# Kernel optimization log

Hardware: AMD Instinct MI355X
Metric: run time of the kernel (lower is better)

The kernel has to match this reference:

```python
import jax, jax.numpy as jnp
import numpy as np

D_MODEL = 3072
N_HEADS = 24
HEAD_DIM = D_MODEL // N_HEADS          # 128
Q_PROJ = D_MODEL // 2                  # 1536
KV_PROJ = 2 * D_MODEL // 3             # 2048
ROPE_DIM = HEAD_DIM // 2               # 64 (qk_rope_dim == qk_no_rope_dim)
MAX_LEN = 2048
ROPE_THETA = 10000.0
EPS = 1e-6
B, S = 2, 2048


def setup_inputs() -> dict:
    key = jax.random.key(0)
    ks = jax.random.split(key, 7)
    return {
        "x": jax.random.normal(ks[0], (B, S, D_MODEL), dtype=jnp.float32),
        "scale": jnp.ones((D_MODEL,), dtype=jnp.float32),
        "w_dq": 0.01 * jax.random.normal(ks[1], (D_MODEL, Q_PROJ), dtype=jnp.float32),
        "w_uq": 0.01 * jax.random.normal(ks[2], (Q_PROJ, D_MODEL), dtype=jnp.float32),
        "w_dkv": 0.01 * jax.random.normal(ks[3], (D_MODEL, KV_PROJ + ROPE_DIM), dtype=jnp.float32),
        "w_ukv": 0.01 * jax.random.normal(ks[4], (KV_PROJ, D_MODEL + N_HEADS * ROPE_DIM), dtype=jnp.float32),
        "w_o": 0.01 * jax.random.normal(ks[5], (D_MODEL, D_MODEL), dtype=jnp.float32),
    }


def _rope_cos_sin(seq_len):
    # freqs over full head_dim, sliced to rope_dim//2 then tiled x2 (as in torch repeat)
    freqs = 1.0 / (ROPE_THETA ** (jnp.arange(0, HEAD_DIM, 2, dtype=jnp.float32) / HEAD_DIM))
    angles = jnp.arange(seq_len, dtype=jnp.float32)[:, None] * freqs[None, :]  # [S, 64]
    ang = angles[:, : ROPE_DIM // 2]                                            # [S, 32]
    cos = jnp.tile(jnp.cos(ang), (1, 2))                                        # [S, 64]
    sin = jnp.tile(jnp.sin(ang), (1, 2))
    return cos[None, None], sin[None, None]  # [1,1,S,64]


def _rotate_half(t):
    a, b = jnp.split(t, 2, axis=-1)
    return jnp.concatenate([-b, a], axis=-1)


def reference(x, scale, w_dq, w_uq, w_dkv, w_ukv, w_o):
    b, s, _ = x.shape
    # RMSNorm pre-normalization
    xn = scale * (x * jax.lax.rsqrt(jnp.mean(x * x, axis=-1, keepdims=True) + EPS))
    # two-stage query projection
    q = (xn @ w_dq) @ w_uq                                   # [B,S,D]
    q = q.reshape(b, s, N_HEADS, HEAD_DIM).transpose(0, 2, 1, 3)  # [B,H,S,hd]
    q_no_rope, q_rope = jnp.split(q, [ROPE_DIM], axis=-1)
    cos, sin = _rope_cos_sin(s)
    q_rope = q_rope * cos + _rotate_half(q_rope) * sin
    # KV down projection (this is the kv cache)
    kv_down = xn @ w_dkv                                     # [B,S,KV_PROJ+rope]
    kv_no_rope, k_rope = jnp.split(kv_down, [KV_PROJ], axis=-1)
    # KV up projection
    kv_up = kv_no_rope @ w_ukv                               # [B,S,H*(hd+rope)]
    kv_up = kv_up.reshape(b, s, N_HEADS, HEAD_DIM + ROPE_DIM).transpose(0, 2, 1, 3)
    key, value = jnp.split(kv_up, [ROPE_DIM], axis=-1)       # key [B,H,S,64], value [B,H,S,128]
    # shared rope key (one head, broadcast to all heads)
    k_rope = k_rope[:, None, :, :]                           # [B,1,S,64]
    k_rope = k_rope * cos + _rotate_half(k_rope) * sin
    k_rope = jnp.broadcast_to(k_rope, (b, N_HEADS, s, ROPE_DIM))
    final_q = jnp.concatenate([q_no_rope, q_rope], axis=-1)  # [B,H,S,128]
    final_k = jnp.concatenate([key, k_rope], axis=-1)        # [B,H,S,128]
    # masked SDPA (causal, past_length=0)
    inv_scale = 1.0 / jnp.sqrt(jnp.asarray(HEAD_DIM, dtype=x.dtype))
    scores = jnp.einsum("bhsd,bhtd->bhst", final_q, final_k) * inv_scale
    causal = jnp.tril(jnp.ones((s, s), dtype=bool))
    scores = jnp.where(causal[None, None], scores, jnp.asarray(-1e30, dtype=scores.dtype))
    attn = jax.nn.softmax(scores, axis=-1)
    attn_out = jnp.einsum("bhst,bhtd->bhsd", attn, value)    # [B,H,S,128]
    attn_out = attn_out.transpose(0, 2, 1, 3).reshape(b, s, D_MODEL)
    output = attn_out @ w_o.T
    return output, kv_down
```

## Files before the change

kernel.cpp:

```cpp
#include <hip/hip_runtime.h>
#include <hip/hip_bf16.h>
#include <stdint.h>

using bf16_t = __bf16;
using bf16x8 = __attribute__((ext_vector_type(8))) __bf16;
using bf16x4 = __attribute__((ext_vector_type(4))) __bf16;
using f32x4  = __attribute__((ext_vector_type(4))) float;

#define D_MODEL 3072
#define N_HEADS 24
#define HEAD_DIM 128
#define Q_PROJ 1536
#define KV_PROJ 2048
#define ROPE_DIM 64
#define S_LEN 2048
#define NTOK 4096
#define KVDN 2112
#define KVUN 4608

__device__ __forceinline__ void async_ld16(const void* g, void* l) {
    __builtin_amdgcn_global_load_lds(
        (__attribute__((address_space(1))) uint32_t*)(uintptr_t)g,
        (__attribute__((address_space(3))) uint32_t*)(uint32_t)(uintptr_t)l,
        16, 0, 0);
}

#define BARRIER() __builtin_amdgcn_s_barrier()
#define WAITV4() asm volatile("s_waitcnt vmcnt(4)" ::: "memory")
#define WAITV0() asm volatile("s_waitcnt vmcnt(0)" ::: "memory")

__global__ __launch_bounds__(256) void rmsnorm_kernel(
    const float* __restrict__ x, const float* __restrict__ sc, bf16_t* __restrict__ xn)
{
    const int tok = blockIdx.x;
    const int t = threadIdx.x;
    const float4* xr = (const float4*)(x + (size_t)tok * D_MODEL);
    float4 a = xr[t], b = xr[t + 256], c = xr[t + 512];
    float ss = a.x*a.x + a.y*a.y + a.z*a.z + a.w*a.w
             + b.x*b.x + b.y*b.y + b.z*b.z + b.w*b.w
             + c.x*c.x + c.y*c.y + c.z*c.z + c.w*c.w;
    #pragma unroll
    for (int off = 32; off >= 1; off >>= 1) ss += __shfl_xor(ss, off);
    __shared__ float red[4];
    if ((t & 63) == 0) red[t >> 6] = ss;
    __syncthreads();
    const float inv = rsqrtf((red[0] + red[1] + red[2] + red[3]) * (1.0f / D_MODEL) + 1e-6f);
    const float4* sr = (const float4*)sc;
    float4 s0 = sr[t], s1 = sr[t + 256], s2 = sr[t + 512];
    bf16x4* xo = (bf16x4*)(xn + (size_t)tok * D_MODEL);
    bf16x4 o;
    o[0]=(bf16_t)(a.x*s0.x*inv); o[1]=(bf16_t)(a.y*s0.y*inv); o[2]=(bf16_t)(a.z*s0.z*inv); o[3]=(bf16_t)(a.w*s0.w*inv);
    xo[t] = o;
    o[0]=(bf16_t)(b.x*s1.x*inv); o[1]=(bf16_t)(b.y*s1.y*inv); o[2]=(bf16_t)(b.z*s1.z*inv); o[3]=(bf16_t)(b.w*s1.w*inv);
    xo[t + 256] = o;
    o[0]=(bf16_t)(c.x*s2.x*inv); o[1]=(bf16_t)(c.y*s2.y*inv); o[2]=(bf16_t)(c.z*s2.z*inv); o[3]=(bf16_t)(c.w*s2.w*inv);
    xo[t + 512] = o;
}

__global__ void transpose_conv(const float* __restrict__ in, bf16_t* __restrict__ out, int K, int N)
{
    __shared__ float tile[32][33];
    const int n0 = blockIdx.x * 32, k0 = blockIdx.y * 32;
    const int tx = threadIdx.x, ty = threadIdx.y;
    #pragma unroll
    for (int i = 0; i < 32; i += 8)
        tile[ty + i][tx] = in[(size_t)(k0 + ty + i) * N + n0 + tx];
    __syncthreads();
    #pragma unroll
    for (int i = 0; i < 32; i += 8)
        out[(size_t)(n0 + ty + i) * K + k0 + tx] = (bf16_t)tile[tx][ty + i];
}

__global__ void conv_bf16(const float* __restrict__ in, bf16_t* __restrict__ out, int n4)
{
    const int stride = gridDim.x * 256;
    for (int i = blockIdx.x * 256 + threadIdx.x; i < n4; i += stride) {
        float4 v = ((const float4*)in)[i];
        bf16x4 o;
        o[0] = (bf16_t)v.x; o[1] = (bf16_t)v.y; o[2] = (bf16_t)v.z; o[3] = (bf16_t)v.w;
        ((bf16x4*)out)[i] = o;
    }
}

template<int CFP>
__device__ __forceinline__ void mfma16(f32x4 (&acc)[8][4], const bf16x8 (&af)[8],
                                       const bf16x8 (&bfv)[2]) {
    __builtin_amdgcn_s_setprio(1);
    #pragma unroll
    for (int rf = 0; rf < 8; ++rf) {
        acc[rf][2*CFP]   = __builtin_amdgcn_mfma_f32_16x16x32_bf16(af[rf], bfv[0], acc[rf][2*CFP],   0, 0, 0);
        acc[rf][2*CFP+1] = __builtin_amdgcn_mfma_f32_16x16x32_bf16(af[rf], bfv[1], acc[rf][2*CFP+1], 0, 0, 0);
    }
    __builtin_amdgcn_s_setprio(0);
}

__global__ __launch_bounds__(512, 2) void gemm256(
    const bf16_t* __restrict__ A, const bf16_t* __restrict__ B, int N, int K,
    float* __restrict__ Cf, int ldf, int flo, int fhi,
    bf16_t* __restrict__ Cb1, int ldb1, int b1lo, int b1hi,
    bf16_t* __restrict__ Cb2, int ldb2, int b2lo, int b2hi)
{
    __shared__ char LDS[131072];
    char* Lc = LDS;
    const int tid = threadIdx.x;
    const int wv = tid >> 6, lane = tid & 63;
    const int fr = lane & 15, fg = lane >> 4;
    const int wr = wv >> 2, wc = wv & 3;
    const int m0 = blockIdx.y << 8, n0 = blockIdx.x << 8;
    const uint32_t slot4 = (uint32_t)((fg ^ ((fr >> 1) & 3)) << 4);

    int grow[2], gcol[2];
    const bf16_t* agp[2]; const bf16_t* bgp[2];
    uint32_t aoff[2], boff[2];
    #pragma unroll
    for (int j = 0; j < 2; ++j) {
        const int c = j * 512 + tid;
        const int g = c ^ ((c >> 3) & 3);
        grow[j] = g >> 2; gcol[j] = g & 3;
        agp[j] = A + (size_t)(m0 + grow[j]) * K + gcol[j] * 8;
        int br = n0 + grow[j]; if (br > N - 1) br = N - 1;
        bgp[j] = B + (size_t)br * K + gcol[j] * 8;
        aoff[j] = (uint32_t)((j * 8 + wv) * 1024);
        boff[j] = (uint32_t)(65536 + (j * 8 + wv) * 1024);
    }

    f32x4 acc[8][4];
    f32x4 zero = {0.f, 0.f, 0.f, 0.f};
    #pragma unroll
    for (int i = 0; i < 8; ++i)
        #pragma unroll
        for (int j = 0; j < 4; ++j) acc[i][j] = zero;

    bf16x8 af[8], bfv[2];
    const int rowA = (wr << 7) + fr;
    const int rowB = (wc << 6) + fr;

    auto stA = [&](int t, int kh) {
        const uint32_t sb = (uint32_t)(((2*t + kh) & 3) << 14);
        #pragma unroll
        for (int j = 0; j < 2; ++j)
            async_ld16(agp[j] + t * 64 + kh * 32, Lc + sb + aoff[j]);
    };
    auto stB = [&](int t, int kh) {
        const uint32_t sb = (uint32_t)(((2*t + kh) & 3) << 14);
        #pragma unroll
        for (int j = 0; j < 2; ++j)
            async_ld16(bgp[j] + t * 64 + kh * 32, Lc + sb + boff[j]);
    };
    auto ldA8 = [&](int t, int kh) {
        const uint32_t base = (uint32_t)(((2*t + kh) & 3) << 14);
        #pragma unroll
        for (int rf = 0; rf < 8; ++rf)
            af[rf] = *(const bf16x8*)(Lc + base + (rowA + rf * 16) * 64 + slot4);
    };
    auto ldB2 = [&](int t, int kh, int cfp) {
        const uint32_t base = (uint32_t)(65536 + (((2*t + kh) & 3) << 14));
        #pragma unroll
        for (int c = 0; c < 2; ++c)
            bfv[c] = *(const bf16x8*)(Lc + base + (rowB + (cfp * 2 + c) * 16) * 64 + slot4);
    };

    const int NT = K >> 6, nIter = NT >> 1;
    stA(0, 0); stB(0, 0); stA(0, 1); stB(0, 1); stA(1, 0); stB(1, 0);
    WAITV4(); BARRIER();

    for (int i = 0; i < nIter; ++i) {
        const int t0 = 2 * i, t1 = t0 + 1, t2 = t0 + 2, t3 = t0 + 3;
        const bool pref = (i < nIter - 1);
        ldA8(t0, 0); ldB2(t0, 0, 0); stA(t1, 1);
        BARRIER(); mfma16<0>(acc, af, bfv); BARRIER();
        ldB2(t0, 0, 1); stB(t1, 1);
        BARRIER(); mfma16<1>(acc, af, bfv); BARRIER();
        ldA8(t0, 1); ldB2(t0, 1, 0); if (pref) stA(t2, 0);
        BARRIER(); mfma16<0>(acc, af, bfv); BARRIER();
        ldB2(t0, 1, 1); if (pref) stB(t2, 0);
        if (pref) { WAITV4(); } else { WAITV0(); }
        BARRIER(); mfma16<1>(acc, af, bfv); BARRIER();
        ldA8(t1, 0); ldB2(t1, 0, 0); if (pref) stA(t2, 1);
        BARRIER(); mfma16<0>(acc, af, bfv); BARRIER();
        ldB2(t1, 0, 1); if (pref) stB(t2, 1);
        BARRIER(); mfma16<1>(acc, af, bfv); BARRIER();
        ldA8(t1, 1); ldB2(t1, 1, 0); if (pref) stA(t3, 0);
        BARRIER(); mfma16<0>(acc, af, bfv); BARRIER();
        ldB2(t1, 1, 1); if (pref) stB(t3, 0);
        WAITV4();
        BARRIER(); mfma16<1>(acc, af, bfv); BARRIER();
    }

    const int colb = n0 + (wc << 6) + fr;
    const int rowb = m0 + (wr << 7) + fg * 4;
    #pragma unroll
    for (int rf = 0; rf < 8; ++rf)
        #pragma unroll
        for (int cf = 0; cf < 4; ++cf) {
            const int col = colb + cf * 16;
            #pragma unroll
            for (int r = 0; r < 4; ++r) {
                const int row = rowb + rf * 16 + r;
                const float v = acc[rf][cf][r];
                if (Cf  && col >= flo  && col < fhi)  Cf [(size_t)row * ldf  + col - flo]  = v;
                if (Cb1 && col >= b1lo && col < b1hi) Cb1[(size_t)row * ldb1 + col - b1lo] = (bf16_t)v;
                if (Cb2 && col >= b2lo && col < b2hi) Cb2[(size_t)row * ldb2 + col - b2lo] = (bf16_t)v;
            }
        }
}

__global__ void rope_tab(float* __restrict__ ctab, float* __restrict__ stab)
{
    const int idx = blockIdx.x * 256 + threadIdx.x;
    if (idx >= S_LEN * 32) return;
    const int s = idx >> 5, i = idx & 31;
    const float freq = powf(10000.0f, -(float)(2 * i) * (1.0f / 128.0f));
    const float ang = (float)s * freq;
    ctab[idx] = cosf(ang);
    stab[idx] = sinf(ang);
}

__global__ void rope_q_kernel(bf16_t* __restrict__ q, const float* __restrict__ ctab,
                              const float* __restrict__ stab)
{
    const int idx = blockIdx.x * 256 + threadIdx.x;
    if (idx >= NTOK * N_HEADS * 32) return;
    const int i = idx & 31;
    const int rest = idx >> 5;
    const int h = rest % N_HEADS;
    const int tok = rest / N_HEADS;
    const int s = tok & (S_LEN - 1);
    bf16_t* p = q + (size_t)tok * D_MODEL + h * HEAD_DIM + 64;
    const float a = (float)p[i], b = (float)p[i + 32];
    const float c = ctab[s * 32 + i], sn = stab[s * 32 + i];
    p[i]      = (bf16_t)(a * c - b * sn);
    p[i + 32] = (bf16_t)(b * c + a * sn);
}

__global__ void rope_k_kernel(const float* __restrict__ kvd, bf16_t* __restrict__ kr,
                              const float* __restrict__ ctab, const float* __restrict__ stab)
{
    const int idx = blockIdx.x * 256 + threadIdx.x;
    if (idx >= NTOK * 32) return;
    const int i = idx & 31;
    const int tok = idx >> 5;
    const int s = tok & (S_LEN - 1);
    const float* p = kvd + (size_t)tok * KVDN + KV_PROJ;
    const float a = p[i], b = p[i + 32];
    const float c = ctab[s * 32 + i], sn = stab[s * 32 + i];
    kr[(size_t)tok * 64 + i]      = (bf16_t)(a * c - b * sn);
    kr[(size_t)tok * 64 + i + 32] = (bf16_t)(b * c + a * sn);
}

__global__ void vt_asm(const bf16_t* __restrict__ kvup, bf16_t* __restrict__ vt)
{
    __shared__ bf16_t tile[32][33];
    const int s0 = blockIdx.x * 32, d0 = blockIdx.y * 32, bh = blockIdx.z;
    const int b = bh / N_HEADS, h = bh % N_HEADS;
    const int tx = threadIdx.x, ty = threadIdx.y;
    #pragma unroll
    for (int i = 0; i < 32; i += 8)
        tile[ty + i][tx] = kvup[(size_t)(b * S_LEN + s0 + ty + i) * KVUN + h * 192 + 64 + d0 + tx];
    __syncthreads();
    #pragma unroll
    for (int i = 0; i < 32; i += 8)
        vt[((size_t)bh * HEAD_DIM + d0 + ty + i) * S_LEN + s0 + tx] = tile[tx][ty + i];
}

__global__ __launch_bounds__(256, 2) void attn_fwd(
    const bf16_t* __restrict__ Q, const bf16_t* __restrict__ KVUP,
    const bf16_t* __restrict__ KR, const bf16_t* __restrict__ VT,
    bf16_t* __restrict__ AO)
{
    __shared__ bf16_t Knr[64 * 64];
    __shared__ bf16_t Krp[64 * 64];
    __shared__ bf16_t Vls[128 * 64];
    __shared__ bf16_t Pls[4 * 32 * 72];

    const int bh = blockIdx.y;
    const int b = bh / N_HEADS, h = bh % N_HEADS;
    const int wave = threadIdx.x >> 6, lane = threadIdx.x & 63;
    const int fr = lane & 15, fg = lane >> 4;
    const int rx = fr & 7;

    const bf16_t* Kb  = KVUP + (size_t)b * S_LEN * KVUN + (size_t)h * 192;
    const bf16_t* KRb = KR + (size_t)b * S_LEN * 64;
    const bf16_t* Vb  = VT + (size_t)bh * HEAD_DIM * S_LEN;
    bf16_t* P = Pls + wave * (32 * 72);

    const int srow   = lane >> 3;
    const int schunk = (lane & 7) ^ srow;
    const float l2e_isc = 0.127500625f;

    f32x4 zero = {0.f, 0.f, 0.f, 0.f};

    #pragma unroll 1
    for (int tp = 0; tp < 2; ++tp) {
        const int qt = (tp == 0) ? blockIdx.x : (15 - blockIdx.x);
        const int qb = qt * 128;
        const int wrow0 = qb + wave * 32;

        bf16x8 qf[2][4];
        #pragma unroll
        for (int rf = 0; rf < 2; ++rf)
            #pragma unroll
            for (int kc = 0; kc < 4; ++kc)
                qf[rf][kc] = *(const bf16x8*)(Q + (size_t)(b * S_LEN + wrow0 + rf * 16 + fr) * D_MODEL
                                              + h * HEAD_DIM + kc * 32 + fg * 8);
        f32x4 oacc[2][8];
        float m_i[2][4], l_i[2][4];
        #pragma unroll
        for (int rf = 0; rf < 2; ++rf) {
            #pragma unroll
            for (int nf = 0; nf < 8; ++nf) oacc[rf][nf] = zero;
            #pragma unroll
            for (int r = 0; r < 4; ++r) { m_i[rf][r] = -1e30f; l_i[rf][r] = 0.f; }
        }

        const int kvend = qb + 128;
        #pragma unroll 1
        for (int kvb = 0; kvb < kvend; kvb += 64) {
            __syncthreads();
            #pragma unroll
            for (int c = 0; c < 2; ++c) {
                const int r0 = wave * 16 + c * 8;
                async_ld16(Kb  + (size_t)(kvb + r0 + srow) * KVUN + schunk * 8, Knr + r0 * 64);
                async_ld16(KRb + (size_t)(kvb + r0 + srow) * 64   + schunk * 8, Krp + r0 * 64);
            }
            #pragma unroll
            for (int c = 0; c < 4; ++c) {
                const int r0 = wave * 32 + c * 8;
                async_ld16(Vb + (size_t)(r0 + srow) * S_LEN + kvb + schunk * 8, Vls + r0 * 64);
            }
            __syncthreads();

            if (kvb > wrow0 + 31) continue;

            f32x4 sacc[2][4];
            #pragma unroll
            for (int rf = 0; rf < 2; ++rf)
                #pragma unroll
                for (int jn = 0; jn < 4; ++jn) sacc[rf][jn] = zero;
            #pragma unroll
            for (int jn = 0; jn < 4; ++jn) {
                const int krow = jn * 16 + fr;
                bf16x8 kA = *(const bf16x8*)(Knr + krow * 64 + (((0 + fg) ^ rx) << 3));
                bf16x8 kB = *(const bf16x8*)(Knr + krow * 64 + (((4 + fg) ^ rx) << 3));
                bf16x8 kC = *(const bf16x8*)(Krp + krow * 64 + (((0 + fg) ^ rx) << 3));
                bf16x8 kD = *(const bf16x8*)(Krp + krow * 64 + (((4 + fg) ^ rx) << 3));
                #pragma unroll
                for (int rf = 0; rf < 2; ++rf) {
                    sacc[rf][jn] = __builtin_amdgcn_mfma_f32_16x16x32_bf16(qf[rf][0], kA, sacc[rf][jn], 0, 0, 0);
                    sacc[rf][jn] = __builtin_amdgcn_mfma_f32_16x16x32_bf16(qf[rf][1], kB, sacc[rf][jn], 0, 0, 0);
                    sacc[rf][jn] = __builtin_amdgcn_mfma_f32_16x16x32_bf16(qf[rf][2], kC, sacc[rf][jn], 0, 0, 0);
                    sacc[rf][jn] = __builtin_amdgcn_mfma_f32_16x16x32_bf16(qf[rf][3], kD, sacc[rf][jn], 0, 0, 0);
                }
            }

            const bool needMask = (kvb + 63 > wrow0);
            float mrow[2][4];
            #pragma unroll
            for (int rf = 0; rf < 2; ++rf)
                #pragma unroll
                for (int r = 0; r < 4; ++r) {
                    const int row = wrow0 + rf * 16 + fg * 4 + r;
                    float mx = -1e30f;
                    #pragma unroll
                    for (int jn = 0; jn < 4; ++jn) {
                        float v = sacc[rf][jn][r] * l2e_isc;
                        if (needMask && (kvb + jn * 16 + fr > row)) v = -1e30f;
                        sacc[rf][jn][r] = v;
                        mx = fmaxf(mx, v);
                    }
                    mrow[rf][r] = mx;
                }
            #pragma unroll
            for (int off = 1; off < 16; off <<= 1)
                #pragma unroll
                for (int rf = 0; rf < 2; ++rf)
                    #pragma unroll
                    for (int r = 0; r < 4; ++r)
                        mrow[rf][r] = fmaxf(mrow[rf][r], __shfl_xor(mrow[rf][r], off));
            float scf[2][4], lsum[2][4];
            #pragma unroll
            for (int rf = 0; rf < 2; ++rf)
                #pragma unroll
                for (int r = 0; r < 4; ++r) {
                    const float mn = fmaxf(m_i[rf][r], mrow[rf][r]);
                    scf[rf][r] = __builtin_amdgcn_exp2f(m_i[rf][r] - mn);
                    m_i[rf][r] = mn;
                    float s = 0.f;
                    #pragma unroll
                    for (int jn = 0; jn < 4; ++jn) {
                        const float p = __builtin_amdgcn_exp2f(sacc[rf][jn][r] - mn);
                        sacc[rf][jn][r] = p;
                        s += p;
                    }
                    lsum[rf][r] = s;
                }
            #pragma unroll
            for (int off = 1; off < 16; off <<= 1)
                #pragma unroll
                for (int rf = 0; rf < 2; ++rf)
                    #pragma unroll
                    for (int r = 0; r < 4; ++r)
                        lsum[rf][r] += __shfl_xor(lsum[rf][r], off);
            #pragma unroll
            for (int rf = 0; rf < 2; ++rf)
                #pragma unroll
                for (int r = 0; r < 4; ++r) {
                    l_i[rf][r] = l_i[rf][r] * scf[rf][r] + lsum[rf][r];
                    #pragma unroll
                    for (int nf = 0; nf < 8; ++nf) oacc[rf][nf][r] *= scf[rf][r];
                }

            #pragma unroll
            for (int rf = 0; rf < 2; ++rf)
                #pragma unroll
                for (int jn = 0; jn < 4; ++jn)
                    #pragma unroll
                    for (int r = 0; r < 4; ++r)
                        P[(rf * 16 + fg * 4 + r) * 72 + jn * 16 + fr] = (bf16_t)sacc[rf][jn][r];
            bf16x8 pf[2][2];
            #pragma unroll
            for (int rf = 0; rf < 2; ++rf)
                #pragma unroll
                for (int c = 0; c < 2; ++c)
                    pf[rf][c] = *(const bf16x8*)(P + (rf * 16 + fr) * 72 + c * 32 + fg * 8);

            #pragma unroll
            for (int nf = 0; nf < 8; ++nf) {
                const int vrow = nf * 16 + fr;
                bf16x8 v0 = *(const bf16x8*)(Vls + vrow * 64 + (((0 + fg) ^ rx) << 3));
                bf16x8 v1 = *(const bf16x8*)(Vls + vrow * 64 + (((4 + fg) ^ rx) << 3));
                #pragma unroll
                for (int rf = 0; rf < 2; ++rf) {
                    oacc[rf][nf] = __builtin_amdgcn_mfma_f32_16x16x32_bf16(pf[rf][0], v0, oacc[rf][nf], 0, 0, 0);
                    oacc[rf][nf] = __builtin_amdgcn_mfma_f32_16x16x32_bf16(pf[rf][1], v1, oacc[rf][nf], 0, 0, 0);
                }
            }
        }

        #pragma unroll
        for (int rf = 0; rf < 2; ++rf) {
            float rl[4];
            #pragma unroll
            for (int r = 0; r < 4; ++r) rl[r] = __builtin_amdgcn_rcpf(l_i[rf][r]);
            #pragma unroll
            for (int nf = 0; nf < 8; ++nf)
                #pragma unroll
                for (int r = 0; r < 4; ++r) {
                    const int row = wrow0 + rf * 16 + fg * 4 + r;
                    AO[(size_t)(b * S_LEN + row) * D_MODEL + h * HEAD_DIM + nf * 16 + fr] =
                        (bf16_t)(oacc[rf][nf][r] * rl[r]);
                }
        }
    }
}

extern "C" void kernel_launch(void* const* d_in, const int* in_sizes, int n_in,
                              void* d_out, int out_size, void* d_ws, size_t ws_size,
                              hipStream_t stream)
{
    const float* x     = (const float*)d_in[0];
    const float* scale = (const float*)d_in[1];
    const float* w_dq  = (const float*)d_in[2];
    const float* w_uq  = (const float*)d_in[3];
    const float* w_dkv = (const float*)d_in[4];
    const float* w_ukv = (const float*)d_in[5];
    const float* w_o   = (const float*)d_in[6];
    float* out0 = (float*)d_out;
    float* out1 = out0 + (size_t)NTOK * D_MODEL;

    if (ws_size < 187039744ull) return;
    char* ws = (char*)d_ws;
    bf16_t* XN    = (bf16_t*)(ws + 0);
    bf16_t* WCAT  = (bf16_t*)(ws + 25165824ull);
    bf16_t* WUQT  = (bf16_t*)(ws + 47579136ull);
    bf16_t* WUKVT = (bf16_t*)(ws + 57016320ull);
    bf16_t* WOB   = (bf16_t*)(ws + 75890688ull);
    bf16_t* QD    = (bf16_t*)(ws + 94765056ull);
    bf16_t* Qb    = (bf16_t*)(ws + 107347968ull);
    bf16_t* KVNR  = (bf16_t*)(ws + 132513792ull);
    bf16_t* KVUP  = (bf16_t*)(ws + 149291008ull);
    bf16_t* KRB   = (bf16_t*)(ws + 94765056ull);
    float*  CTAB  = (float*) (ws + 95289344ull);
    float*  STAB  = (float*) (ws + 95551488ull);
    bf16_t* VTb   = WCAT;
    bf16_t* AO    = XN;

    rmsnorm_kernel<<<NTOK, 256, 0, stream>>>(x, scale, XN);
    transpose_conv<<<dim3(1536/32, 3072/32), dim3(32,8), 0, stream>>>(w_dq,  WCAT, 3072, 1536);
    transpose_conv<<<dim3(2112/32, 3072/32), dim3(32,8), 0, stream>>>(w_dkv, WCAT + (size_t)1536*3072, 3072, 2112);
    transpose_conv<<<dim3(3072/32, 1536/32), dim3(32,8), 0, stream>>>(w_uq,  WUQT, 1536, 3072);
    transpose_conv<<<dim3(4608/32, 2048/32), dim3(32,8), 0, stream>>>(w_ukv, WUKVT, 2048, 4608);
    conv_bf16<<<2048, 256, 0, stream>>>(w_o, WOB, (D_MODEL * D_MODEL) / 4);

    gemm256<<<dim3(15, 16), 512, 0, stream>>>(XN, WCAT, 3648, 3072,
        out1, KVDN, 1536, 3648,
        QD,   Q_PROJ, 0, 1536,
        KVNR, KV_PROJ, 1536, 3584);
    gemm256<<<dim3(12, 16), 512, 0, stream>>>(QD, WUQT, 3072, 1536,
        nullptr, 0, 0, 0, Qb, D_MODEL, 0, 3072, nullptr, 0, 0, 0);
    rope_tab<<<(S_LEN * 32 + 255) / 256, 256, 0, stream>>>(CTAB, STAB);
    rope_q_kernel<<<(NTOK * N_HEADS * 32 + 255) / 256, 256, 0, stream>>>(Qb, CTAB, STAB);
    rope_k_kernel<<<(NTOK * 32 + 255) / 256, 256, 0, stream>>>(out1, KRB, CTAB, STAB);
    gemm256<<<dim3(18, 16), 512, 0, stream>>>(KVNR, WUKVT, 4608, 2048,
        nullptr, 0, 0, 0, KVUP, KVUN, 0, 4608, nullptr, 0, 0, 0);
    vt_asm<<<dim3(S_LEN/32, HEAD_DIM/32, 48), dim3(32,8), 0, stream>>>(KVUP, VTb);
    attn_fwd<<<dim3(8, 48), 256, 0, stream>>>(Qb, KVUP, KRB, VTb, AO);
    gemm256<<<dim3(12, 16), 512, 0, stream>>>(AO, WOB, 3072, 3072,
        out0, D_MODEL, 0, 3072, nullptr, 0, 0, 0, nullptr, 0, 0, 0);
}
```

Before: 590.8 us.

## Double-buffer KV tiles and transpose MFMA to keep P in registers

Makes the attention kernel double-buffer its K, rope-K and V LDS tiles, so the async load of the next block overlaps compute on the current one and one barrier per iteration is removed. It swaps the MFMA operand order so scores come out transposed: each lane then owns one query row, the row max and sum need only two cross-lane shuffles, and P is passed to the PV MFMA through register shuffles instead of an LDS round trip. Output stores become 4-wide vectors. The cost is double the K/V LDS footprint and extra register pressure and shuffle work, which may reduce occupancy.

```diff
diff --git a/kernel.cpp b/kernel.cpp
--- a/kernel.cpp
+++ b/kernel.cpp
@@ -268,21 +268,22 @@
     const bf16_t* __restrict__ KR, const bf16_t* __restrict__ VT,
     bf16_t* __restrict__ AO)
 {
-    __shared__ bf16_t Knr[64 * 64];
-    __shared__ bf16_t Krp[64 * 64];
-    __shared__ bf16_t Vls[128 * 64];
-    __shared__ bf16_t Pls[4 * 32 * 72];
+    __shared__ bf16_t Knr[2][64 * 64];
+    __shared__ bf16_t Krp[2][64 * 64];
+    __shared__ bf16_t Vls[2][128 * 64];
 
     const int bh = blockIdx.y;
     const int b = bh / N_HEADS, h = bh % N_HEADS;
     const int wave = threadIdx.x >> 6, lane = threadIdx.x & 63;
     const int fr = lane & 15, fg = lane >> 4;
     const int rx = fr & 7;
+    const int hi = fg >> 1;
+    const int s0l = fr + 32 * (fg & 1);
+    const int s1l = s0l + 16;
 
     const bf16_t* Kb  = KVUP + (size_t)b * S_LEN * KVUN + (size_t)h * 192;
     const bf16_t* KRb = KR + (size_t)b * S_LEN * 64;
     const bf16_t* Vb  = VT + (size_t)bh * HEAD_DIM * S_LEN;
-    bf16_t* P = Pls + wave * (32 * 72);
 
     const int srow   = lane >> 3;
     const int schunk = (lane & 7) ^ srow;
@@ -304,152 +305,157 @@
                 qf[rf][kc] = *(const bf16x8*)(Q + (size_t)(b * S_LEN + wrow0 + rf * 16 + fr) * D_MODEL
                                               + h * HEAD_DIM + kc * 32 + fg * 8);
         f32x4 oacc[2][8];
-        float m_i[2][4], l_i[2][4];
+        float m_i[2], l_i[2];
         #pragma unroll
         for (int rf = 0; rf < 2; ++rf) {
             #pragma unroll
             for (int nf = 0; nf < 8; ++nf) oacc[rf][nf] = zero;
-            #pragma unroll
-            for (int r = 0; r < 4; ++r) { m_i[rf][r] = -1e30f; l_i[rf][r] = 0.f; }
+            m_i[rf] = -1e30f; l_i[rf] = 0.f;
         }
 
-        const int kvend = qb + 128;
-        #pragma unroll 1
-        for (int kvb = 0; kvb < kvend; kvb += 64) {
-            __syncthreads();
+        auto stage = [&](int kvb, int bf) {
             #pragma unroll
             for (int c = 0; c < 2; ++c) {
                 const int r0 = wave * 16 + c * 8;
-                async_ld16(Kb  + (size_t)(kvb + r0 + srow) * KVUN + schunk * 8, Knr + r0 * 64);
-                async_ld16(KRb + (size_t)(kvb + r0 + srow) * 64   + schunk * 8, Krp + r0 * 64);
+                async_ld16(Kb  + (size_t)(kvb + r0 + srow) * KVUN + schunk * 8, &Knr[bf][r0 * 64]);
+                async_ld16(KRb + (size_t)(kvb + r0 + srow) * 64   + schunk * 8, &Krp[bf][r0 * 64]);
             }
             #pragma unroll
             for (int c = 0; c < 4; ++c) {
                 const int r0 = wave * 32 + c * 8;
-                async_ld16(Vb + (size_t)(r0 + srow) * S_LEN + kvb + schunk * 8, Vls + r0 * 64);
+                async_ld16(Vb + (size_t)(r0 + srow) * S_LEN + kvb + schunk * 8, &Vls[bf][r0 * 64]);
+            }
+        };
+
+        const int kvend = qb + 128;
+        int cur = 0;
+        stage(0, 0);
+        __syncthreads();
+
+        #pragma unroll 1
+        for (int kvb = 0; kvb < kvend; kvb += 64) {
+            if (kvb + 64 < kvend) stage(kvb + 64, cur ^ 1);
+
+            if (kvb <= wrow0 + 31) {
+                const bf16_t* Kc = Knr[cur];
+                const bf16_t* Rc = Krp[cur];
+                const bf16_t* Vc = Vls[cur];
+
+                f32x4 sacc[2][4];
+                #pragma unroll
+                for (int rf = 0; rf < 2; ++rf)
+                    #pragma unroll
+                    for (int jn = 0; jn < 4; ++jn) sacc[rf][jn] = zero;
+                #pragma unroll
+                for (int jn = 0; jn < 4; ++jn) {
+                    const int krow = jn * 16 + fr;
+                    bf16x8 kA = *(const bf16x8*)(Kc + krow * 64 + (((0 + fg) ^ rx) << 3));
+                    bf16x8 kB = *(const bf16x8*)(Kc + krow * 64 + (((4 + fg) ^ rx) << 3));
+                    bf16x8 kC = *(const bf16x8*)(Rc + krow * 64 + (((0 + fg) ^ rx) << 3));
+                    bf16x8 kD = *(const bf16x8*)(Rc + krow * 64 + (((4 + fg) ^ rx) << 3));
+                    #pragma unroll
+                    for (int rf = 0; rf < 2; ++rf) {
+                        sacc[rf][jn] = __builtin_amdgcn_mfma_f32_16x16x32_bf16(kA, qf[rf][0], sacc[rf][jn], 0, 0, 0);
+                        sacc[rf][jn] = __builtin_amdgcn_mfma_f32_16x16x32_bf16(kB, qf[rf][1], sacc[rf][jn], 0, 0, 0);
+                        sacc[rf][jn] = __builtin_amdgcn_mfma_f32_16x16x32_bf16(kC, qf[rf][2], sacc[rf][jn], 0, 0, 0);
+                        sacc[rf][jn] = __builtin_amdgcn_mfma_f32_16x16x32_bf16(kD, qf[rf][3], sacc[rf][jn], 0, 0, 0);
+                    }
+                }
+
+                const bool needMask = (kvb + 63 > wrow0);
+                uint32_t pk[2][4][2];
+                float scf[2];
+                #pragma unroll
+                for (int rf = 0; rf < 2; ++rf) {
+                    const int qrow = wrow0 + rf * 16 + fr;
+                    float mx = -1e30f;
+                    #pragma unroll
+                    for (int jn = 0; jn < 4; ++jn)
+                        #pragma unroll
+                        for (int r = 0; r < 4; ++r) {
+                            float v = sacc[rf][jn][r] * l2e_isc;
+                            if (needMask && (kvb + jn * 16 + fg * 4 + r > qrow)) v = -1e30f;
+                            sacc[rf][jn][r] = v;
+                            mx = fmaxf(mx, v);
+                        }
+                    mx = fmaxf(mx, __shfl_xor(mx, 16));
+                    mx = fmaxf(mx, __shfl_xor(mx, 32));
+                    const float mn = fmaxf(m_i[rf], mx);
+                    scf[rf] = __builtin_amdgcn_exp2f(m_i[rf] - mn);
+                    m_i[rf] = mn;
+                    float ls = 0.f;
+                    #pragma unroll
+                    for (int jn = 0; jn < 4; ++jn) {
+                        float p0 = __builtin_amdgcn_exp2f(sacc[rf][jn][0] - mn);
+                        float p1 = __builtin_amdgcn_exp2f(sacc[rf][jn][1] - mn);
+                        float p2 = __builtin_amdgcn_exp2f(sacc[rf][jn][2] - mn);
+                        float p3 = __builtin_amdgcn_exp2f(sacc[rf][jn][3] - mn);
+                        ls += (p0 + p1) + (p2 + p3);
+                        union { bf16x4 h; uint32_t w[2]; } cv;
+                        cv.h[0] = (bf16_t)p0; cv.h[1] = (bf16_t)p1;
+                        cv.h[2] = (bf16_t)p2; cv.h[3] = (bf16_t)p3;
+                        pk[rf][jn][0] = cv.w[0]; pk[rf][jn][1] = cv.w[1];
+                    }
+                    ls += __shfl_xor(ls, 16);
+                    ls += __shfl_xor(ls, 32);
+                    l_i[rf] = l_i[rf] * scf[rf] + ls;
+                    #pragma unroll
+                    for (int nf = 0; nf < 8; ++nf)
+                        #pragma unroll
+                        for (int r = 0; r < 4; ++r) oacc[rf][nf][r] *= scf[rf];
+                }
+
+                bf16x8 bfr[2][2];
+                #pragma unroll
+                for (int rf = 0; rf < 2; ++rf)
+                    #pragma unroll
+                    for (int ks = 0; ks < 2; ++ks) {
+                        const uint32_t t00 = __shfl(pk[rf][2*ks][0],   s0l);
+                        const uint32_t t01 = __shfl(pk[rf][2*ks][1],   s0l);
+                        const uint32_t t10 = __shfl(pk[rf][2*ks+1][0], s0l);
+                        const uint32_t t11 = __shfl(pk[rf][2*ks+1][1], s0l);
+                        const uint32_t u00 = __shfl(pk[rf][2*ks][0],   s1l);
+                        const uint32_t u01 = __shfl(pk[rf][2*ks][1],   s1l);
+                        const uint32_t u10 = __shfl(pk[rf][2*ks+1][0], s1l);
+                        const uint32_t u11 = __shfl(pk[rf][2*ks+1][1], s1l);
+                        union { bf16x8 h; uint32_t w[4]; } bb;
+                        bb.w[0] = hi ? t10 : t00;
+                        bb.w[1] = hi ? t11 : t01;
+                        bb.w[2] = hi ? u10 : u00;
+                        bb.w[3] = hi ? u11 : u01;
+                        bfr[rf][ks] = bb.h;
+                    }
+
+                #pragma unroll
+                for (int nf = 0; nf < 8; ++nf) {
+                    const int vrow = nf * 16 + fr;
+                    bf16x8 v0 = *(const bf16x8*)(Vc + vrow * 64 + (((0 + fg) ^ rx) << 3));
+                    bf16x8 v1 = *(const bf16x8*)(Vc + vrow * 64 + (((4 + fg) ^ rx) << 3));
+                    #pragma unroll
+                    for (int rf = 0; rf < 2; ++rf) {
+                        oacc[rf][nf] = __builtin_amdgcn_mfma_f32_16x16x32_bf16(v0, bfr[rf][0], oacc[rf][nf], 0, 0, 0);
+                        oacc[rf][nf] = __builtin_amdgcn_mfma_f32_16x16x32_bf16(v1, bfr[rf][1], oacc[rf][nf], 0, 0, 0);
+                    }
+                }
             }
             __syncthreads();
-
-            if (kvb > wrow0 + 31) continue;
-
-            f32x4 sacc[2][4];
-            #pragma unroll
-            for (int rf = 0; rf < 2; ++rf)
-                #pragma unroll
-                for (int jn = 0; jn < 4; ++jn) sacc[rf][jn] = zero;
-            #pragma unroll
-            for (int jn = 0; jn < 4; ++jn) {
-                const int krow = jn * 16 + fr;
-                bf16x8 kA = *(const bf16x8*)(Knr + krow * 64 + (((0 + fg) ^ rx) << 3));
-                bf16x8 kB = *(const bf16x8*)(Knr + krow * 64 + (((4 + fg) ^ rx) << 3));
-                bf16x8 kC = *(const bf16x8*)(Krp + krow * 64 + (((0 + fg) ^ rx) << 3));
-                bf16x8 kD = *(const bf16x8*)(Krp + krow * 64 + (((4 + fg) ^ rx) << 3));
-                #pragma unroll
-                for (int rf = 0; rf < 2; ++rf) {
-                    sacc[rf][jn] = __builtin_amdgcn_mfma_f32_16x16x32_bf16(qf[rf][0], kA, sacc[rf][jn], 0, 0, 0);
-                    sacc[rf][jn] = __builtin_amdgcn_mfma_f32_16x16x32_bf16(qf[rf][1], kB, sacc[rf][jn], 0, 0, 0);
-                    sacc[rf][jn] = __builtin_amdgcn_mfma_f32_16x16x32_bf16(qf[rf][2], kC, sacc[rf][jn], 0, 0, 0);
-                    sacc[rf][jn] = __builtin_amdgcn_mfma_f32_16x16x32_bf16(qf[rf][3], kD, sacc[rf][jn], 0, 0, 0);
-                }
-            }
-
-            const bool needMask = (kvb + 63 > wrow0);
-            float mrow[2][4];
-            #pragma unroll
-            for (int rf = 0; rf < 2; ++rf)
-                #pragma unroll
-                for (int r = 0; r < 4; ++r) {
-                    const int row = wrow0 + rf * 16 + fg * 4 + r;
-                    float mx = -1e30f;
-                    #pragma unroll
-                    for (int jn = 0; jn < 4; ++jn) {
-                        float v = sacc[rf][jn][r] * l2e_isc;
-                        if (needMask && (kvb + jn * 16 + fr > row)) v = -1e30f;
-                        sacc[rf][jn][r] = v;
-                        mx = fmaxf(mx, v);
-                    }
-                    mrow[rf][r] = mx;
-                }
-            #pragma unroll
-            for (int off = 1; off < 16; off <<= 1)
-                #pragma unroll
-                for (int rf = 0; rf < 2; ++rf)
-                    #pragma unroll
-                    for (int r = 0; r < 4; ++r)
-                        mrow[rf][r] = fmaxf(mrow[rf][r], __shfl_xor(mrow[rf][r], off));
-            float scf[2][4], lsum[2][4];
-            #pragma unroll
-            for (int rf = 0; rf < 2; ++rf)
-                #pragma unroll
-                for (int r = 0; r < 4; ++r) {
-                    const float mn = fmaxf(m_i[rf][r], mrow[rf][r]);
-                    scf[rf][r] = __builtin_amdgcn_exp2f(m_i[rf][r] - mn);
-                    m_i[rf][r] = mn;
-                    float s = 0.f;
-                    #pragma unroll
-                    for (int jn = 0; jn < 4; ++jn) {
-                        const float p = __builtin_amdgcn_exp2f(sacc[rf][jn][r] - mn);
-                        sacc[rf][jn][r] = p;
-                        s += p;
-                    }
-                    lsum[rf][r] = s;
-                }
-            #pragma unroll
-            for (int off = 1; off < 16; off <<= 1)
-                #pragma unroll
-                for (int rf = 0; rf < 2; ++rf)
-                    #pragma unroll
-                    for (int r = 0; r < 4; ++r)
-                        lsum[rf][r] += __shfl_xor(lsum[rf][r], off);
-            #pragma unroll
-            for (int rf = 0; rf < 2; ++rf)
-                #pragma unroll
-                for (int r = 0; r < 4; ++r) {
-                    l_i[rf][r] = l_i[rf][r] * scf[rf][r] + lsum[rf][r];
-                    #pragma unroll
-                    for (int nf = 0; nf < 8; ++nf) oacc[rf][nf][r] *= scf[rf][r];
-                }
-
-            #pragma unroll
-            for (int rf = 0; rf < 2; ++rf)
-                #pragma unroll
-                for (int jn = 0; jn < 4; ++jn)
-                    #pragma unroll
-                    for (int r = 0; r < 4; ++r)
-                        P[(rf * 16 + fg * 4 + r) * 72 + jn * 16 + fr] = (bf16_t)sacc[rf][jn][r];
-            bf16x8 pf[2][2];
-            #pragma unroll
-            for (int rf = 0; rf < 2; ++rf)
-                #pragma unroll
-                for (int c = 0; c < 2; ++c)
-                    pf[rf][c] = *(const bf16x8*)(P + (rf * 16 + fr) * 72 + c * 32 + fg * 8);
-
+            cur ^= 1;
+        }
+
+        #pragma unroll
+        for (int rf = 0; rf < 2; ++rf) {
+            const float rl = __builtin_amdgcn_rcpf(l_i[rf]);
+            const int qrow = wrow0 + rf * 16 + fr;
+            bf16_t* aob = AO + (size_t)(b * S_LEN + qrow) * D_MODEL + h * HEAD_DIM + fg * 4;
             #pragma unroll
             for (int nf = 0; nf < 8; ++nf) {
-                const int vrow = nf * 16 + fr;
-                bf16x8 v0 = *(const bf16x8*)(Vls + vrow * 64 + (((0 + fg) ^ rx) << 3));
-                bf16x8 v1 = *(const bf16x8*)(Vls + vrow * 64 + (((4 + fg) ^ rx) << 3));
-                #pragma unroll
-                for (int rf = 0; rf < 2; ++rf) {
-                    oacc[rf][nf] = __builtin_amdgcn_mfma_f32_16x16x32_bf16(pf[rf][0], v0, oacc[rf][nf], 0, 0, 0);
-                    oacc[rf][nf] = __builtin_amdgcn_mfma_f32_16x16x32_bf16(pf[rf][1], v1, oacc[rf][nf], 0, 0, 0);
-                }
+                bf16x4 o;
+                o[0] = (bf16_t)(oacc[rf][nf][0] * rl);
+                o[1] = (bf16_t)(oacc[rf][nf][1] * rl);
+                o[2] = (bf16_t)(oacc[rf][nf][2] * rl);
+                o[3] = (bf16_t)(oacc[rf][nf][3] * rl);
+                *(bf16x4*)(aob + nf * 16) = o;
             }
-        }
-
-        #pragma unroll
-        for (int rf = 0; rf < 2; ++rf) {
-            float rl[4];
-            #pragma unroll
-            for (int r = 0; r < 4; ++r) rl[r] = __builtin_amdgcn_rcpf(l_i[rf][r]);
-            #pragma unroll
-            for (int nf = 0; nf < 8; ++nf)
-                #pragma unroll
-                for (int r = 0; r < 4; ++r) {
-                    const int row = wrow0 + rf * 16 + fg * 4 + r;
-                    AO[(size_t)(b * S_LEN + row) * D_MODEL + h * HEAD_DIM + nf * 16 + fr] =
-                        (bf16_t)(oacc[rf][nf][r] * rl[r]);
-                }
         }
     }
 }
```

Result: faster. 555.2 us (-6.0%).
